# Kernel tuning notes

Measured on AMD Instinct MI355X. Metric: run time of the kernel, lower is better.

Reference implementation:

```python
import jax, jax.numpy as jnp
import numpy as np

NORMALIZED_LENGTH = 1.0
LOSS_WEIGHTS = (0.25, 1.0)
EPS = 1e-12  # matches torch F.normalize eps


def setup_inputs() -> dict:
    key = jax.random.key(0)
    k1, k2 = jax.random.split(key)
    x = jax.random.normal(k1, (16, 128, 64, 64), dtype=jnp.float32)
    codebook = jax.random.normal(k2, (1024, 128), dtype=jnp.float32)
    return {"x": x, "codebook": codebook}


def _forward(x, codebook):
    # --- VQCodebook.forward: normalize x along channel dim (dim=1) ---
    # NOTE: the torch source's codebook renormalization uses non-in-place
    # .div/.mul whose results are discarded, so the codebook is unchanged.
    if NORMALIZED_LENGTH > 0:
        nrm = jnp.linalg.norm(x, axis=1, keepdims=True)  # [B,1,H,W]
        x = NORMALIZED_LENGTH * x / jnp.maximum(nrm, EPS)

    B, C, H, W = x.shape
    z = jnp.transpose(x, (0, 2, 3, 1)).reshape(-1, C)  # [N, C], N = B*H*W

    # Pairwise squared L2 distances via ||z||^2 - 2 z c^T + ||c||^2.
    # argmin of squared distance == argmin of distance.
    z2 = jnp.sum(z * z, axis=1, keepdims=True)             # [N, 1]
    c2 = jnp.sum(codebook * codebook, axis=1)              # [K]
    d2 = z2 - 2.0 * jnp.einsum('nc,kc->nk', z, codebook) + c2[None, :]  # [N, K]
    idx = jnp.argmin(d2, axis=1)                           # [N]

    q = codebook[idx]                                      # [N, C]
    q = q.reshape(B, H, W, C).transpose(0, 3, 1, 2)        # [B, C, H, W]

    lw0, lw1 = LOSS_WEIGHTS
    diff_codebook = jax.lax.stop_gradient(x) - q
    diff_commit = x - jax.lax.stop_gradient(q)
    loss0 = lw0 * jnp.mean(jnp.linalg.norm(diff_codebook, axis=1))
    loss1 = lw1 * jnp.mean(jnp.linalg.norm(diff_commit, axis=1))
    return q, loss0, loss1


def reference(x, codebook):
    return _forward(x, codebook)
```

## Files before the change

kernel.cpp:

```cpp
#include <hip/hip_runtime.h>
#include <math.h>

#define K_CODES 1024
#define C_DIM   128
#define HW      4096
#define CHW     (C_DIM*HW)
#define N_POS   65536
#define Q_ELEMS 8388608

#define WS_S    0
#define WS_C2   256
#define WS_IDX  8192


typedef __attribute__((ext_vector_type(8))) short short8;
typedef __attribute__((ext_vector_type(4))) float f32x4;

__device__ __forceinline__ unsigned short f2bf(float f) {
    unsigned u = __float_as_uint(f);
    u += 0x7FFFu + ((u >> 16) & 1u);
    return (unsigned short)(u >> 16);
}

__device__ __forceinline__ void gll16(const void* g, void* l) {
    __builtin_amdgcn_global_load_lds(
        (const __attribute__((address_space(1))) void*)g,
        (__attribute__((address_space(3))) void*)l, 16, 0, 0);
}

__global__ __launch_bounds__(256) void prep_kernel(const float* __restrict__ cb,
                                                   float* __restrict__ ws,
                                                   unsigned short* __restrict__ cbbf) {
    __shared__ __align__(16) unsigned short srow[4][128];
    int t = threadIdx.x;
    int w = t >> 6;
    int l = t & 63;
    int k = blockIdx.x * 4 + w;
    if (blockIdx.x == 0 && t == 0) *(float*)((char*)ws + WS_S) = 0.f;
    float v1 = cb[k * C_DIM + l];
    float v2 = cb[k * C_DIM + 64 + l];
    int c1 = l, c2 = 64 + l;
    srow[w][(((c1 >> 3) ^ (k & 7)) << 3) | (c1 & 7)] = f2bf(v1);
    srow[w][(((c2 >> 3) ^ (k & 7)) << 3) | (c2 & 7)] = f2bf(v2);
    float ss = v1 * v1 + v2 * v2;
    #pragma unroll
    for (int off = 32; off > 0; off >>= 1) ss += __shfl_down(ss, off);
    if (l == 0) ((float*)((char*)ws + WS_C2))[k] = ss;
    __syncthreads();
    if (l < 16) ((uint4*)cbbf)[k * 16 + l] = ((const uint4*)srow[w])[l];
}

__global__ __launch_bounds__(256, 2) void vq_mfma(const float* __restrict__ x,
                                                  const float* __restrict__ cb,
                                                  const unsigned short* __restrict__ cbbf,
                                                  const float* __restrict__ c2w,
                                                  int* __restrict__ idxw,
                                                  float* __restrict__ Sw,
                                                  float* __restrict__ out) {
    __shared__ __align__(16) unsigned short cbuf[2][4][4096];
    __shared__ float mbuf[4][4][16][3];
    __shared__ float nbuf[4][64];
    __shared__ int ibuf[64];

    const int t  = threadIdx.x;
    const int w  = t >> 6;
    const int ln = t & 63;
    const int lp = ln & 15;
    const int q  = ln >> 4;
    const int bid = blockIdx.x;
    const int b   = bid >> 6;
    const int s0  = (bid & 63) << 6;

    const char* gq = (const char*)cbbf + (w << 16);

    {
        const char* gs = gq + (ln << 4);
        char* ld = (char*)&cbuf[0][w][0];
        #pragma unroll
        for (int r = 0; r < 8; ++r) gll16(gs + r * 1024, ld + r * 1024);
    }

    unsigned short* xbuf = &cbuf[1][0][0];
    {
        float ssp = 0.f;
        const float* xgp = x + b * CHW + (w * 32) * HW + s0 + ln;
        #pragma unroll
        for (int g = 0; g < 4; ++g) {
            union { short8 v; unsigned short u[8]; } fu;
            #pragma unroll
            for (int j = 0; j < 8; ++j) {
                float vv = xgp[(g * 8 + j) * HW];
                ssp = fmaf(vv, vv, ssp);
                fu.u[j] = f2bf(vv);
            }
            int col = (w * 4 + g) ^ (ln & 7);
            *(short8*)(xbuf + ln * 128 + col * 8) = fu.v;
        }
        nbuf[w][ln] = ssp;
    }
    __syncthreads();

    float r2v[4];
    #pragma unroll
    for (int pt = 0; pt < 4; ++pt) {
        const int pos = pt * 16 + lp;
        float s01 = nbuf[0][pos] + nbuf[1][pos];
        float s23 = nbuf[2][pos] + nbuf[3][pos];
        float s   = s01 + s23;
        r2v[pt] = -2.0f / fmaxf(sqrtf(s), 1e-12f);
    }

    short8 xf[4][4];
    #pragma unroll
    for (int pt = 0; pt < 4; ++pt)
        #pragma unroll
        for (int cs = 0; cs < 4; ++cs) {
            int col = (4 * cs + q) ^ (lp & 7);
            xf[pt][cs] = *(const short8*)(xbuf + (pt * 16 + lp) * 128 + col * 8);
        }
    asm volatile("s_waitcnt lgkmcnt(0)" ::: "memory");
    __builtin_amdgcn_sched_barrier(0);
    __syncthreads();

    const float FMAX = __uint_as_float(0x7F7FFFFFu);
    float m1[4] = {FMAX, FMAX, FMAX, FMAX};
    float m2[4] = {FMAX, FMAX, FMAX, FMAX};
    float m3[4] = {FMAX, FMAX, FMAX, FMAX};

    asm volatile("s_waitcnt vmcnt(0)" ::: "memory");
    __builtin_amdgcn_sched_barrier(0);

    for (int i = 0; i < 8; ++i) {
        if (i < 7) {
            asm volatile("s_waitcnt lgkmcnt(0)" ::: "memory");
            const char* gs = gq + (i + 1) * 8192 + (ln << 4);
            char* ld = (char*)&cbuf[(i + 1) & 1][w][0];
            #pragma unroll
            for (int r = 0; r < 8; ++r) gll16(gs + r * 1024, ld + r * 1024);
        }

        const int k0 = (w << 8) + (i << 5);
        const unsigned short* cbp = &cbuf[i & 1][w][0];

        f32x4 acc[2][4];
        #pragma unroll
        for (int ct = 0; ct < 2; ++ct)
            #pragma unroll
            for (int pt = 0; pt < 4; ++pt) acc[ct][pt] = 0;

        #pragma unroll
        for (int cs = 0; cs < 4; ++cs) {
            short8 ah[2];
            #pragma unroll
            for (int ct = 0; ct < 2; ++ct) {
                int g = (16 * ct + lp) * 16 + ((4 * cs + q) ^ (lp & 7));
                ah[ct] = *(const short8*)(cbp + g * 8);
            }
            #pragma unroll
            for (int ct = 0; ct < 2; ++ct)
                #pragma unroll
                for (int pt = 0; pt < 4; ++pt)
                    acc[ct][pt] = __builtin_amdgcn_mfma_f32_16x16x32_bf16(
                        ah[ct], xf[pt][cs], acc[ct][pt], 0, 0, 0);
        }

        #pragma unroll
        for (int ct = 0; ct < 2; ++ct) {
            float4 c2vv = *(const float4*)(c2w + k0 + 16 * ct + 4 * q);
            float c2a[4] = {c2vv.x, c2vv.y, c2vv.z, c2vv.w};
            const int kb0 = k0 + 16 * ct + 4 * q;
            #pragma unroll
            for (int pt = 0; pt < 4; ++pt) {
                #pragma unroll
                for (int reg = 0; reg < 4; ++reg) {
                    float s = fmaf(r2v[pt], acc[ct][pt][reg], c2a[reg]);
                    unsigned pb = (__float_as_uint(s) & 0xFFFFFC00u) |
                                  (unsigned)(kb0 + reg);
                    float u  = __uint_as_float(pb);
                    float t3 = __builtin_amdgcn_fmed3f(m2[pt], m3[pt], u);
                    float t2 = __builtin_amdgcn_fmed3f(m1[pt], m2[pt], u);
                    m1[pt] = fminf(m1[pt], u); m2[pt] = t2; m3[pt] = t3;
                }
            }
        }

        if (i < 7) {
            asm volatile("s_waitcnt vmcnt(0)" ::: "memory");
            __builtin_amdgcn_sched_barrier(0);
        }
    }

    #pragma unroll
    for (int d = 16; d <= 32; d <<= 1) {
        #pragma unroll
        for (int pt = 0; pt < 4; ++pt) {
            float o1 = __shfl_xor(m1[pt], d), o2 = __shfl_xor(m2[pt], d),
                  o3 = __shfl_xor(m3[pt], d);
            float u, t2, t3;
            u = o1; t3 = __builtin_amdgcn_fmed3f(m2[pt], m3[pt], u);
            t2 = __builtin_amdgcn_fmed3f(m1[pt], m2[pt], u);
            m1[pt] = fminf(m1[pt], u); m2[pt] = t2; m3[pt] = t3;
            u = o2; t3 = __builtin_amdgcn_fmed3f(m2[pt], m3[pt], u);
            t2 = __builtin_amdgcn_fmed3f(m1[pt], m2[pt], u);
            m1[pt] = fminf(m1[pt], u); m2[pt] = t2; m3[pt] = t3;
            u = o3; t3 = __builtin_amdgcn_fmed3f(m2[pt], m3[pt], u);
            t2 = __builtin_amdgcn_fmed3f(m1[pt], m2[pt], u);
            m1[pt] = fminf(m1[pt], u); m2[pt] = t2; m3[pt] = t3;
        }
    }

    if (ln < 16) {
        #pragma unroll
        for (int pt = 0; pt < 4; ++pt) {
            mbuf[w][pt][lp][0] = m1[pt];
            mbuf[w][pt][lp][1] = m2[pt];
            mbuf[w][pt][lp][2] = m3[pt];
        }
    }

    float xr2[2][32];
    if (w < 2) {
        #pragma unroll
        for (int ptl = 0; ptl < 2; ++ptl) {
            const int pt = 2 * w + ptl;
            const float* xgp = x + b * CHW + s0 + pt * 16 + lp;
            #pragma unroll
            for (int cs = 0; cs < 4; ++cs)
                #pragma unroll
                for (int j = 0; j < 8; ++j)
                    xr2[ptl][cs * 8 + j] = xgp[(32 * cs + 8 * q + j) * HW];
        }
    }
    __syncthreads();

    if (w < 2) {
        float lsum = 0.f;
        #pragma unroll
        for (int ptl = 0; ptl < 2; ++ptl) {
            const int pt = 2 * w + ptl;
            float M1 = FMAX, M2 = FMAX, M3 = FMAX;
            #pragma unroll
            for (int ww = 0; ww < 4; ++ww)
                #pragma unroll
                for (int c = 0; c < 3; ++c) {
                    float u  = mbuf[ww][pt][lp][c];
                    float t3 = __builtin_amdgcn_fmed3f(M2, M3, u);
                    float t2 = __builtin_amdgcn_fmed3f(M1, M2, u);
                    M1 = fminf(M1, u); M2 = t2; M3 = t3;
                }
            int ks[3] = {(int)(__float_as_uint(M1) & 1023u),
                         (int)(__float_as_uint(M2) & 1023u),
                         (int)(__float_as_uint(M3) & 1023u)};

            const float* xr = xr2[ptl];

            float dots[3];
            #pragma unroll
            for (int jj = 0; jj < 3; ++jj) {
                const float* crow = cb + ks[jj] * C_DIM + 8 * q;
                float p = 0.f;
                #pragma unroll
                for (int cs = 0; cs < 4; ++cs) {
                    float4 a0 = *(const float4*)(crow + 32 * cs);
                    float4 a1 = *(const float4*)(crow + 32 * cs + 4);
                    p = fmaf(xr[cs*8+0], a0.x, p); p = fmaf(xr[cs*8+1], a0.y, p);
                    p = fmaf(xr[cs*8+2], a0.z, p); p = fmaf(xr[cs*8+3], a0.w, p);
                    p = fmaf(xr[cs*8+4], a1.x, p); p = fmaf(xr[cs*8+5], a1.y, p);
                    p = fmaf(xr[cs*8+6], a1.z, p); p = fmaf(xr[cs*8+7], a1.w, p);
                }
                p += __shfl_xor(p, 16);
                p += __shfl_xor(p, 32);
                dots[jj] = p;
            }
            float sb = fmaf(r2v[pt], dots[0], c2w[ks[0]]); int kb = ks[0];
            float s2 = fmaf(r2v[pt], dots[1], c2w[ks[1]]);
            if (s2 < sb || (s2 == sb && ks[1] < kb)) { sb = s2; kb = ks[1]; }
            float s3 = fmaf(r2v[pt], dots[2], c2w[ks[2]]);
            if (s3 < sb || (s3 == sb && ks[2] < kb)) { sb = s3; kb = ks[2]; }

            if (ln < 16) {
                idxw[bid * 64 + pt * 16 + lp] = kb;
                ibuf[pt * 16 + lp] = kb;
            }
            lsum += sqrtf(fmaxf(1.0f + sb, 0.f));
        }
        #pragma unroll
        for (int off = 32; off > 0; off >>= 1) lsum += __shfl_down(lsum, off);
        if (ln == 0) atomicAdd(Sw, 0.25f * lsum);
    }

    __syncthreads();
    if (b != 0) {
        const int row = ibuf[ln];
        const float4* cbr = (const float4*)cb + row * 32;
        float* ob = out + b * CHW + s0 + ln;
        #pragma unroll
        for (int c4 = w * 8; c4 < w * 8 + 8; ++c4) {
            float4 v = cbr[c4];
            float* o = ob + (c4 * 4) * HW;
            o[0]      = v.x;
            o[HW]     = v.y;
            o[2 * HW] = v.z;
            o[3 * HW] = v.w;
        }
    }
}

__global__ void write_q0(const float* __restrict__ cb,
                         const int* __restrict__ idxw,
                         const float* __restrict__ ws,
                         float* __restrict__ out) {
    int id = blockIdx.x * 256 + threadIdx.x;
    int s  = id & 4095;
    int c4 = id >> 12;
    int row = idxw[s];
    float4 v = ((const float4*)cb)[row * 32 + c4];
    float* o = out + (c4 * 4) * HW + s;
    o[0]      = v.x;
    o[HW]     = v.y;
    o[2 * HW] = v.z;
    o[3 * HW] = v.w;
    if (id == 0) {
        float S = *(const float*)((const char*)ws + WS_S);
        float m = S / (float)N_POS;
        out[Q_ELEMS]     = 0.25f * m;
        out[Q_ELEMS + 1] = m;
    }
}

extern "C" void kernel_launch(void* const* d_in, const int* in_sizes, int n_in,
                              void* d_out, int out_size, void* d_ws, size_t ws_size,
                              hipStream_t stream) {
    const float* x  = (const float*)d_in[0];
    const float* cb = (const float*)d_in[1];
    float* out = (float*)d_out;
    float* ws  = (float*)d_ws;

    const float* c2w = (const float*)((const char*)d_ws + WS_C2);
    int*  idxw = (int*)((char*)d_ws + WS_IDX);
    float* Sw  = (float*)((char*)d_ws + WS_S);
    unsigned short* cbbf = (unsigned short*)d_out;

    prep_kernel<<<K_CODES / 4, 256, 0, stream>>>(cb, ws, cbbf);
    vq_mfma    <<<N_POS / 64, 256, 0, stream>>>(x, cb, cbbf, c2w, idxw, Sw, out);
    write_q0   <<<512, 256, 0, stream>>>(cb, idxw, ws, out);
}
```

Measured before the change: 66.46 us.

## Switch codebook staging to triple-buffered half-size chunks with partial vmcnt waits

```diff
diff --git a/kernel.cpp b/kernel.cpp
--- a/kernel.cpp
+++ b/kernel.cpp
@@ -57,7 +57,7 @@
                                                   int* __restrict__ idxw,
                                                   float* __restrict__ Sw,
                                                   float* __restrict__ out) {
-    __shared__ __align__(16) unsigned short cbuf[2][4][4096];
+    __shared__ __align__(16) unsigned short cbuf[3][4][2048];
     __shared__ float mbuf[4][4][16][3];
     __shared__ float nbuf[4][64];
     __shared__ int ibuf[64];
@@ -75,12 +75,15 @@
 
     {
         const char* gs = gq + (ln << 4);
-        char* ld = (char*)&cbuf[0][w][0];
-        #pragma unroll
-        for (int r = 0; r < 8; ++r) gll16(gs + r * 1024, ld + r * 1024);
-    }
-
-    unsigned short* xbuf = &cbuf[1][0][0];
+        char* l0 = (char*)&cbuf[0][w][0];
+        char* l1 = (char*)&cbuf[1][w][0];
+        #pragma unroll
+        for (int r = 0; r < 4; ++r) gll16(gs + r * 1024, l0 + r * 1024);
+        #pragma unroll
+        for (int r = 0; r < 4; ++r) gll16(gs + 4096 + r * 1024, l1 + r * 1024);
+    }
+
+    unsigned short* xbuf = &cbuf[2][0][0];
     {
         float ssp = 0.f;
         const float* xgp = x + b * CHW + (w * 32) * HW + s0 + ln;
@@ -127,53 +130,47 @@
     float m2[4] = {FMAX, FMAX, FMAX, FMAX};
     float m3[4] = {FMAX, FMAX, FMAX, FMAX};
 
-    asm volatile("s_waitcnt vmcnt(0)" ::: "memory");
-    __builtin_amdgcn_sched_barrier(0);
-
-    for (int i = 0; i < 8; ++i) {
-        if (i < 7) {
+    for (int i = 0; i < 16; ++i) {
+        const int k0 = (w << 8) + (i << 4);
+        float4 c2vv = *(const float4*)(c2w + k0 + 4 * q);
+
+        if (i < 14) {
             asm volatile("s_waitcnt lgkmcnt(0)" ::: "memory");
-            const char* gs = gq + (i + 1) * 8192 + (ln << 4);
-            char* ld = (char*)&cbuf[(i + 1) & 1][w][0];
-            #pragma unroll
-            for (int r = 0; r < 8; ++r) gll16(gs + r * 1024, ld + r * 1024);
-        }
-
-        const int k0 = (w << 8) + (i << 5);
-        const unsigned short* cbp = &cbuf[i & 1][w][0];
-
-        f32x4 acc[2][4];
-        #pragma unroll
-        for (int ct = 0; ct < 2; ++ct)
-            #pragma unroll
-            for (int pt = 0; pt < 4; ++pt) acc[ct][pt] = 0;
+            const char* gs = gq + (i + 2) * 4096 + (ln << 4);
+            char* ld = (char*)&cbuf[(i + 2) % 3][w][0];
+            #pragma unroll
+            for (int r = 0; r < 4; ++r) gll16(gs + r * 1024, ld + r * 1024);
+        }
+
+        if (i < 14)       asm volatile("s_waitcnt vmcnt(9)" ::: "memory");
+        else if (i == 14) asm volatile("s_waitcnt vmcnt(5)" ::: "memory");
+        else              asm volatile("s_waitcnt vmcnt(1)" ::: "memory");
+        __builtin_amdgcn_sched_barrier(0);
+
+        const unsigned short* cbp = &cbuf[i % 3][w][0];
+
+        f32x4 acc[4];
+        #pragma unroll
+        for (int pt = 0; pt < 4; ++pt) acc[pt] = 0;
 
         #pragma unroll
         for (int cs = 0; cs < 4; ++cs) {
-            short8 ah[2];
-            #pragma unroll
-            for (int ct = 0; ct < 2; ++ct) {
-                int g = (16 * ct + lp) * 16 + ((4 * cs + q) ^ (lp & 7));
-                ah[ct] = *(const short8*)(cbp + g * 8);
-            }
-            #pragma unroll
-            for (int ct = 0; ct < 2; ++ct)
-                #pragma unroll
-                for (int pt = 0; pt < 4; ++pt)
-                    acc[ct][pt] = __builtin_amdgcn_mfma_f32_16x16x32_bf16(
-                        ah[ct], xf[pt][cs], acc[ct][pt], 0, 0, 0);
-        }
-
-        #pragma unroll
-        for (int ct = 0; ct < 2; ++ct) {
-            float4 c2vv = *(const float4*)(c2w + k0 + 16 * ct + 4 * q);
+            int g = lp * 16 + ((4 * cs + q) ^ (lp & 7));
+            short8 ah = *(const short8*)(cbp + g * 8);
+            #pragma unroll
+            for (int pt = 0; pt < 4; ++pt)
+                acc[pt] = __builtin_amdgcn_mfma_f32_16x16x32_bf16(
+                    ah, xf[pt][cs], acc[pt], 0, 0, 0);
+        }
+
+        {
             float c2a[4] = {c2vv.x, c2vv.y, c2vv.z, c2vv.w};
-            const int kb0 = k0 + 16 * ct + 4 * q;
+            const int kb0 = k0 + 4 * q;
             #pragma unroll
             for (int pt = 0; pt < 4; ++pt) {
                 #pragma unroll
                 for (int reg = 0; reg < 4; ++reg) {
-                    float s = fmaf(r2v[pt], acc[ct][pt][reg], c2a[reg]);
+                    float s = fmaf(r2v[pt], acc[pt][reg], c2a[reg]);
                     unsigned pb = (__float_as_uint(s) & 0xFFFFFC00u) |
                                   (unsigned)(kb0 + reg);
                     float u  = __uint_as_float(pb);
@@ -182,11 +179,6 @@
                     m1[pt] = fminf(m1[pt], u); m2[pt] = t2; m3[pt] = t3;
                 }
             }
-        }
-
-        if (i < 7) {
-            asm volatile("s_waitcnt vmcnt(0)" ::: "memory");
-            __builtin_amdgcn_sched_barrier(0);
         }
     }
 
```

Result: faster. 64.93 us (median of 2 runs) (-2.3%).
